# Kernel optimization log

Hardware: AMD Instinct MI355X
Metric: run time of the kernel (lower is better)

The kernel has to match this reference:

```python
import jax, jax.numpy as jnp
import numpy as np

N = 100000      # nodes
E = 1600000     # edges (avg degree 16)
NFEAT = 256
HIDDEN = 256
C = 4           # channels
PC = HIDDEN // C  # per-channel dim = 64
NCLASS = 4
EPS = 1e-12


def setup_inputs() -> dict:
    key = jax.random.key(0)
    ks = jax.random.split(key, 12)
    x = jax.random.normal(ks[0], (N, NFEAT), dtype=jnp.float32)
    row = jax.random.randint(ks[1], (E,), 0, N, dtype=jnp.int64)
    col = jax.random.randint(ks[2], (E,), 0, N, dtype=jnp.int64)
    s = lambda fan_in: 1.0 / np.sqrt(fan_in)
    # NeiborAssigner: Linear(2*nfeat, C) -> Linear(C, C)
    asg_W1 = jax.random.normal(ks[3], (C, 2 * NFEAT), dtype=jnp.float32) * s(2 * NFEAT)
    asg_b1 = jnp.zeros((C,), dtype=jnp.float32)
    asg_W2 = jax.random.normal(ks[4], (C, C), dtype=jnp.float32) * s(C)
    asg_b2 = jnp.zeros((C,), dtype=jnp.float32)
    # DisenLayer: per-channel Linear(nfeat, PC) and conv Linear(PC, PC, bias=False)
    lin_W = jax.random.normal(ks[5], (C, PC, NFEAT), dtype=jnp.float32) * s(NFEAT)
    lin_b = jax.random.normal(ks[6], (C, PC), dtype=jnp.float32) * 0.01
    conv_W = jax.random.normal(ks[7], (C, PC, PC), dtype=jnp.float32) * s(PC)
    bias = jax.random.normal(ks[8], (C, PC), dtype=jnp.float32) * 0.01
    # classifier Linear(hidden, nclass)
    cls_W = jax.random.normal(ks[9], (NCLASS, HIDDEN), dtype=jnp.float32) * s(HIDDEN)
    cls_b = jnp.zeros((NCLASS,), dtype=jnp.float32)
    return {"x": x, "row": row, "col": col,
            "asg_W1": asg_W1, "asg_b1": asg_b1, "asg_W2": asg_W2, "asg_b2": asg_b2,
            "lin_W": lin_W, "lin_b": lin_b, "conv_W": conv_W, "bias": bias,
            "cls_W": cls_W, "cls_b": cls_b}


def reference(x, row, col, asg_W1, asg_b1, asg_W2, asg_b2,
              lin_W, lin_b, conv_W, bias, cls_W, cls_b):
    # --- NeiborAssigner on detached features ---
    xd = jax.lax.stop_gradient(x)
    # cat([x[col], x[row]]) @ W1.T  ==  x[col]@W1a.T + x[row]@W1b.T  (project per node first)
    W1a, W1b = asg_W1[:, :NFEAT], asg_W1[:, NFEAT:]
    proj_a = xd @ W1a.T          # [N, C]
    proj_b = xd @ W1b.T          # [N, C]
    h1 = proj_a[col] + proj_b[row] + asg_b1       # [E, C]
    h2 = h1 @ asg_W2.T + asg_b2                    # [E, C]
    edge_weight = jax.nn.softmax(h2, axis=1)       # [E, C]

    # --- DisenLayer (single layer, layer_num=2) ---
    # per-channel reduce:  z_k = lin_k(x);  c_k = z_k @ conv_W_k.T
    z = jnp.einsum('nf,kpf->nkp', x, lin_W) + lin_b[None]   # [N, C, PC]
    c = jnp.einsum('nkp,kqp->nkq', z, conv_W)               # [N, C, PC]
    # weighted sparse propagate: out[row] += edge_weight[:,k] * c[col]
    msg = c[col] * edge_weight[:, :, None]                  # [E, C, PC]
    out = jax.ops.segment_sum(msg, row, num_segments=N)     # [N, C, PC]
    out = out + bias[None]                                  # per-channel bias
    # F.normalize(p=2, dim=1) per channel
    nrm = jnp.sqrt(jnp.sum(out * out, axis=-1, keepdims=True))
    out = out / jnp.maximum(nrm, EPS)
    h = out.reshape(N, HIDDEN)                              # channel concat
    # dropout is identity in eval mode

    # --- classifier ---
    logits = h @ cls_W.T + cls_b                            # [N, nclass]
    return (h, logits)
```

## Files before the change

### kernel.cpp

```cpp
#include <hip/hip_runtime.h>
#include <hip/hip_bf16.h>

#define N_NODES 100000
#define N_EDGES 1600000
#define BCAP    64
#define EPS     1e-12f

typedef __bf16 bf16x8 __attribute__((ext_vector_type(8)));
typedef float  f32x4  __attribute__((ext_vector_type(4)));

__device__ __forceinline__ unsigned short f2bf(float f){
    union { float f; unsigned int i; } v; v.f = f;
    unsigned int x = v.i;
    return (unsigned short)((x + 0x7fffu + ((x >> 16) & 1u)) >> 16);
}
__device__ __forceinline__ float bits2f(unsigned int u){
    union { unsigned int i; float f; } v; v.i = u; return v.f;
}

__global__ void k_init(int* __restrict__ deg,
                       const float* __restrict__ lin_W,
                       const float* __restrict__ lin_b,
                       const float* __restrict__ conv_W,
                       __bf16* __restrict__ Mbf,
                       float* __restrict__ dvec,
                       const float* __restrict__ asg_W1,
                       const float* __restrict__ x,
                       float* __restrict__ proj_a,
                       float* __restrict__ proj_b){
    int b = blockIdx.x;
    int t = threadIdx.x;
    if (b < 391){
        int i = b * 256 + t;
        if (i < N_NODES) deg[i] = 0;
    } else if (b < 647){
        int id = (b - 391) * 256 + t;
        int f  = id & 255;
        int o  = id >> 8;
        int k  = o >> 6;
        const float* cw = conv_W + o * 64;
        const float* lw = lin_W + k * 64 * 256 + f;
        float s = 0.f;
        #pragma unroll 8
        for (int p = 0; p < 64; ++p) s += cw[p] * lw[p * 256];
        Mbf[id] = (__bf16)s;
        if (f == 0){
            const float* lb = lin_b + k * 64;
            float d = 0.f;
            for (int p = 0; p < 64; ++p) d += lb[p] * cw[p];
            dvec[o] = d;
        }
    } else {
        int p = b - 647;
        int lane = t & 63, wv = t >> 6;
        int nb = p * 128 + wv * 32;
        int l15 = lane & 15, quad = lane >> 4;
        f32x4 accp[2];
        accp[0] = f32x4{0.f, 0.f, 0.f, 0.f};
        accp[1] = f32x4{0.f, 0.f, 0.f, 0.f};
        const float* xg[2];
        #pragma unroll
        for (int mi = 0; mi < 2; ++mi){
            int row = nb + mi * 16 + l15;
            if (row >= N_NODES) row = N_NODES - 1;
            xg[mi] = x + (size_t)row * 256 + quad * 8;
        }
        const float* wrow = asg_W1;
        if (l15 < 4)      wrow = asg_W1 + l15 * 512;
        else if (l15 < 8) wrow = asg_W1 + (l15 - 4) * 512 + 256;
        bool wz = (l15 >= 8);
        for (int k0 = 0; k0 < 256; k0 += 32){
            bf16x8 a[2];
            #pragma unroll
            for (int mi = 0; mi < 2; ++mi){
                float4 lo = *(const float4*)(xg[mi] + k0);
                float4 hi = *(const float4*)(xg[mi] + k0 + 4);
                a[mi][0] = (__bf16)lo.x; a[mi][1] = (__bf16)lo.y;
                a[mi][2] = (__bf16)lo.z; a[mi][3] = (__bf16)lo.w;
                a[mi][4] = (__bf16)hi.x; a[mi][5] = (__bf16)hi.y;
                a[mi][6] = (__bf16)hi.z; a[mi][7] = (__bf16)hi.w;
            }
            bf16x8 bw;
            if (!wz){
                float4 lo = *(const float4*)(wrow + k0 + quad * 8);
                float4 hi = *(const float4*)(wrow + k0 + quad * 8 + 4);
                bw[0] = (__bf16)lo.x; bw[1] = (__bf16)lo.y;
                bw[2] = (__bf16)lo.z; bw[3] = (__bf16)lo.w;
                bw[4] = (__bf16)hi.x; bw[5] = (__bf16)hi.y;
                bw[6] = (__bf16)hi.z; bw[7] = (__bf16)hi.w;
            } else {
                bw[0] = (__bf16)0.f; bw[1] = (__bf16)0.f; bw[2] = (__bf16)0.f; bw[3] = (__bf16)0.f;
                bw[4] = (__bf16)0.f; bw[5] = (__bf16)0.f; bw[6] = (__bf16)0.f; bw[7] = (__bf16)0.f;
            }
            accp[0] = __builtin_amdgcn_mfma_f32_16x16x32_bf16(a[0], bw, accp[0], 0, 0, 0);
            accp[1] = __builtin_amdgcn_mfma_f32_16x16x32_bf16(a[1], bw, accp[1], 0, 0, 0);
        }
        if (l15 < 8){
            #pragma unroll
            for (int mi = 0; mi < 2; ++mi){
                int nrow = nb + mi * 16 + quad * 4;
                #pragma unroll
                for (int r = 0; r < 4; ++r){
                    int node = nrow + r;
                    if (node < N_NODES){
                        float v = accp[mi][r];
                        if (l15 < 4) proj_a[node * 4 + l15] = v;
                        else         proj_b[node * 4 + (l15 - 4)] = v;
                    }
                }
            }
        }
    }
}

__global__ __launch_bounds__(256, 4) void k_ge(const float* __restrict__ x,
                                               const __bf16* __restrict__ Mbf,
                                               const float* __restrict__ dvec,
                                               __bf16* __restrict__ c,
                                               const void* __restrict__ row_raw,
                                               const void* __restrict__ col_raw,
                                               const float* __restrict__ proj_a,
                                               const float* __restrict__ proj_b,
                                               const float* __restrict__ asg_b1,
                                               const float* __restrict__ asg_W2,
                                               const float* __restrict__ asg_b2,
                                               int* __restrict__ deg,
                                               int4* __restrict__ bucket){
    __shared__ int s_is64;
    int b = blockIdx.x;
    int t = threadIdx.x;
    if (b % 5 == 0){
        int gid = b / 5;
        int lane = t & 63, wv = t >> 6;
        int wm = wv & 1, wn = wv >> 1;
        int nb = gid * 64 + wm * 32;
        int ob = wn * 128;
        int l15 = lane & 15, quad = lane >> 4;
        f32x4 acc[2][8];
        #pragma unroll
        for (int mi = 0; mi < 2; ++mi)
            #pragma unroll
            for (int ni = 0; ni < 8; ++ni) acc[mi][ni] = f32x4{0.f, 0.f, 0.f, 0.f};
        const float* xg[2];
        #pragma unroll
        for (int mi = 0; mi < 2; ++mi){
            int row = nb + mi * 16 + l15;
            if (row >= N_NODES) row = N_NODES - 1;
            xg[mi] = x + (size_t)row * 256 + quad * 8;
        }
        for (int k0 = 0; k0 < 256; k0 += 32){
            bf16x8 a[2];
            #pragma unroll
            for (int mi = 0; mi < 2; ++mi){
                float4 lo = *(const float4*)(xg[mi] + k0);
                float4 hi = *(const float4*)(xg[mi] + k0 + 4);
                a[mi][0] = (__bf16)lo.x; a[mi][1] = (__bf16)lo.y;
                a[mi][2] = (__bf16)lo.z; a[mi][3] = (__bf16)lo.w;
                a[mi][4] = (__bf16)hi.x; a[mi][5] = (__bf16)hi.y;
                a[mi][6] = (__bf16)hi.z; a[mi][7] = (__bf16)hi.w;
            }
            #pragma unroll
            for (int ni = 0; ni < 8; ++ni){
                bf16x8 bb = *(const bf16x8*)(Mbf + (size_t)(ob + ni * 16 + l15) * 256 + k0 + quad * 8);
                acc[0][ni] = __builtin_amdgcn_mfma_f32_16x16x32_bf16(a[0], bb, acc[0][ni], 0, 0, 0);
                acc[1][ni] = __builtin_amdgcn_mfma_f32_16x16x32_bf16(a[1], bb, acc[1][ni], 0, 0, 0);
            }
        }
        #pragma unroll
        for (int ni = 0; ni < 8; ++ni){
            int o = ob + ni * 16 + l15;
            float dv = dvec[o];
            #pragma unroll
            for (int mi = 0; mi < 2; ++mi){
                int nrow = nb + mi * 16 + quad * 4;
                #pragma unroll
                for (int r = 0; r < 4; ++r){
                    int node = nrow + r;
                    if (node < N_NODES) c[(size_t)node * 256 + o] = (__bf16)(acc[mi][ni][r] + dv);
                }
            }
        }
    } else {
        int eid = b - b / 5 - 1;
        if (t == 0) s_is64 = 1;
        __syncthreads();
        unsigned v = ((const unsigned*)row_raw)[2 * t + 1] | ((const unsigned*)col_raw)[2 * t + 1];
        if (v) s_is64 = 0;
        __syncthreads();

        int e = eid * 256 + t;
        if (e >= N_EDGES) return;
        int r, cl;
        if (s_is64){
            r  = (int)((const long long*)row_raw)[e];
            cl = (int)((const long long*)col_raw)[e];
        } else {
            r  = ((const int*)row_raw)[e];
            cl = ((const int*)col_raw)[e];
        }
        float4 pa = *(const float4*)(proj_a + (size_t)cl * 4);
        float4 pb = *(const float4*)(proj_b + (size_t)r * 4);
        float h1[4];
        h1[0] = pa.x + pb.x + asg_b1[0];
        h1[1] = pa.y + pb.y + asg_b1[1];
        h1[2] = pa.z + pb.z + asg_b1[2];
        h1[3] = pa.w + pb.w + asg_b1[3];
        float h2[4];
        #pragma unroll
        for (int i = 0; i < 4; ++i){
            float s = asg_b2[i];
            #pragma unroll
            for (int j = 0; j < 4; ++j) s += asg_W2[i * 4 + j] * h1[j];
            h2[i] = s;
        }
        float m = fmaxf(fmaxf(h2[0], h2[1]), fmaxf(h2[2], h2[3]));
        float e0 = __expf(h2[0] - m), e1 = __expf(h2[1] - m);
        float e2 = __expf(h2[2] - m), e3 = __expf(h2[3] - m);
        float inv = 1.f / (e0 + e1 + e2 + e3);
        unsigned b0 = f2bf(e0 * inv), b1 = f2bf(e1 * inv);
        unsigned b2 = f2bf(e2 * inv), b3 = f2bf(e3 * inv);
        int4 rec;
        rec.x = cl;
        rec.y = (int)(b0 | (b1 << 16));
        rec.z = (int)(b2 | (b3 << 16));
        rec.w = 0;
        int pos = atomicAdd(&deg[r], 1);
        if (pos < BCAP) bucket[(size_t)r * BCAP + pos] = rec;
    }
}

__global__ __launch_bounds__(256) void k_node(const __bf16* __restrict__ c,
                                              const int* __restrict__ deg,
                                              const int4* __restrict__ bucket,
                                              const float* __restrict__ bias,
                                              const float* __restrict__ cls_W,
                                              const float* __restrict__ cls_b,
                                              float* __restrict__ out_h,
                                              float* __restrict__ out_logits){
    int wv = __builtin_amdgcn_readfirstlane((int)(threadIdx.x >> 6));
    int l  = threadIdx.x & 63;
    int n  = blockIdx.x * 4 + wv;
    int k2 = l >> 4;

    float4 bi = *(const float4*)(bias  + l * 4);
    float4 w0 = *(const float4*)(cls_W + 0 * 256 + l * 4);
    float4 w1 = *(const float4*)(cls_W + 1 * 256 + l * 4);
    float4 w2 = *(const float4*)(cls_W + 2 * 256 + l * 4);
    float4 w3 = *(const float4*)(cls_W + 3 * 256 + l * 4);

    int dn = deg[n]; if (dn > BCAP) dn = BCAP;
    const int4* rec = bucket + (size_t)n * BCAP;
    const __bf16* cb = c + (size_t)l * 4;

    bool hi2 = (k2 & 2) != 0;
    bool odd = (k2 & 1) != 0;

    float a0 = 0.f, a1 = 0.f, a2 = 0.f, a3 = 0.f;
    #pragma unroll 4
    for (int i = 0; i < dn; ++i){
        int4 rc = rec[i];
        int  ww = hi2 ? rc.z : rc.y;
        unsigned wb = odd ? ((unsigned)ww & 0xffff0000u) : ((unsigned)ww << 16);
        float w = bits2f(wb);
        uint2 vv = *(const uint2*)(cb + (size_t)rc.x * 256);
        a0 += w * bits2f(vv.x << 16);
        a1 += w * bits2f(vv.x & 0xffff0000u);
        a2 += w * bits2f(vv.y << 16);
        a3 += w * bits2f(vv.y & 0xffff0000u);
    }
    a0 += bi.x; a1 += bi.y; a2 += bi.z; a3 += bi.w;

    float ss = a0 * a0 + a1 * a1 + a2 * a2 + a3 * a3;
    ss += __shfl_xor(ss, 1);
    ss += __shfl_xor(ss, 2);
    ss += __shfl_xor(ss, 4);
    ss += __shfl_xor(ss, 8);
    float nrm = fmaxf(sqrtf(ss), EPS);
    float h0 = a0 / nrm, h1 = a1 / nrm, h2 = a2 / nrm, h3 = a3 / nrm;
    *(float4*)(out_h + (size_t)n * 256 + l * 4) = make_float4(h0, h1, h2, h3);

    float p0 = h0 * w0.x + h1 * w0.y + h2 * w0.z + h3 * w0.w;
    float p1 = h0 * w1.x + h1 * w1.y + h2 * w1.z + h3 * w1.w;
    float p2 = h0 * w2.x + h1 * w2.y + h2 * w2.z + h3 * w2.w;
    float p3 = h0 * w3.x + h1 * w3.y + h2 * w3.z + h3 * w3.w;
    #pragma unroll
    for (int off = 1; off < 64; off <<= 1){
        p0 += __shfl_xor(p0, off);
        p1 += __shfl_xor(p1, off);
        p2 += __shfl_xor(p2, off);
        p3 += __shfl_xor(p3, off);
    }
    if (l == 0){
        float4 lg = make_float4(p0 + cls_b[0], p1 + cls_b[1],
                                p2 + cls_b[2], p3 + cls_b[3]);
        *(float4*)(out_logits + (size_t)n * 4) = lg;
    }
}

extern "C" void kernel_launch(void* const* d_in, const int* in_sizes, int n_in,
                              void* d_out, int out_size, void* d_ws, size_t ws_size,
                              hipStream_t stream){
    const float* x       = (const float*)d_in[0];
    const void*  row_raw = d_in[1];
    const void*  col_raw = d_in[2];
    const float* asg_W1  = (const float*)d_in[3];
    const float* asg_b1  = (const float*)d_in[4];
    const float* asg_W2  = (const float*)d_in[5];
    const float* asg_b2  = (const float*)d_in[6];
    const float* lin_W   = (const float*)d_in[7];
    const float* lin_b   = (const float*)d_in[8];
    const float* conv_W  = (const float*)d_in[9];
    const float* bias    = (const float*)d_in[10];
    const float* cls_W   = (const float*)d_in[11];
    const float* cls_b   = (const float*)d_in[12];

    char* ws = (char*)d_ws;
    size_t off = 0;
    auto alloc = [&](size_t bytes) -> void* {
        void* p = ws + off;
        off += (bytes + 255) & ~(size_t)255;
        return p;
    };
    __bf16* c      = (__bf16*)alloc((size_t)N_NODES * 256 * 2);
    int4*   bucket = (int4*)alloc((size_t)N_NODES * BCAP * 16);
    float*  proj_a = (float*)alloc((size_t)N_NODES * 4 * 4);
    float*  proj_b = (float*)alloc((size_t)N_NODES * 4 * 4);
    __bf16* Mbf    = (__bf16*)alloc(65536 * 2);
    float*  dvec   = (float*)alloc(256 * 4);
    int*    deg    = (int*)alloc((size_t)N_NODES * 4);

    float* out_h = (float*)d_out;
    float* out_l = out_h + (size_t)N_NODES * 256;

    hipLaunchKernelGGL(k_init, dim3(647 + (N_NODES + 127) / 128), dim3(256), 0, stream,
                       deg, lin_W, lin_b, conv_W, Mbf, dvec, asg_W1, x, proj_a, proj_b);
    hipLaunchKernelGGL(k_ge, dim3(7813), dim3(256), 0, stream,
                       x, (const __bf16*)Mbf, dvec, c,
                       row_raw, col_raw, proj_a, proj_b, asg_b1, asg_W2, asg_b2,
                       deg, bucket);
    hipLaunchKernelGGL(k_node, dim3(N_NODES / 4), dim3(256), 0, stream,
                       c, deg, bucket, bias, cls_W, cls_b, out_h, out_l);
}
```

Before: 496.8 us.

## Stage x tile in double-buffered LDS and pre-swizzle weight matrix for MFMA loads

The GEMM branch of k_ge now loads each 64-row x tile once per block, converts it to bf16 and stores it in a double-buffered shared-memory tile. This replaces the old scheme where the two waves sharing rows each re-read x from global memory. The next k-slice is prefetched while the MFMAs run. The combined weight matrix is written by k_init in an MFMA-fragment order, so each lane's B load is contiguous and coalesced. The cost is LDS usage and a block barrier per k-step, in a kernel that also carries the edge-processing blocks.

```diff
diff --git a/kernel.cpp b/kernel.cpp
--- a/kernel.cpp
+++ b/kernel.cpp
@@ -22,7 +22,7 @@
                        const float* __restrict__ lin_W,
                        const float* __restrict__ lin_b,
                        const float* __restrict__ conv_W,
-                       __bf16* __restrict__ Mbf,
+                       __bf16* __restrict__ Mp,
                        float* __restrict__ dvec,
                        const float* __restrict__ asg_W1,
                        const float* __restrict__ x,
@@ -43,7 +43,8 @@
         float s = 0.f;
         #pragma unroll 8
         for (int p = 0; p < 64; ++p) s += cw[p] * lw[p * 256];
-        Mbf[id] = (__bf16)s;
+        size_t idx = ((((size_t)(o >> 4) * 8 + (f >> 5)) * 64) + ((f >> 3) & 3) * 16 + (o & 15)) * 8 + (f & 7);
+        Mp[idx] = (__bf16)s;
         if (f == 0){
             const float* lb = lin_b + k * 64;
             float d = 0.f;
@@ -113,8 +114,9 @@
     }
 }
 
+#define ASTRIDE 40
 __global__ __launch_bounds__(256, 4) void k_ge(const float* __restrict__ x,
-                                               const __bf16* __restrict__ Mbf,
+                                               const __bf16* __restrict__ Mp,
                                                const float* __restrict__ dvec,
                                                __bf16* __restrict__ c,
                                                const void* __restrict__ row_raw,
@@ -126,6 +128,7 @@
                                                const float* __restrict__ asg_b2,
                                                int* __restrict__ deg,
                                                int4* __restrict__ bucket){
+    __shared__ __align__(16) __bf16 sA[2][64][ASTRIDE];
     __shared__ int s_is64;
     int b = blockIdx.x;
     int t = threadIdx.x;
@@ -133,46 +136,59 @@
         int gid = b / 5;
         int lane = t & 63, wv = t >> 6;
         int wm = wv & 1, wn = wv >> 1;
-        int nb = gid * 64 + wm * 32;
-        int ob = wn * 128;
+        int nb = gid * 64;
         int l15 = lane & 15, quad = lane >> 4;
         f32x4 acc[2][8];
         #pragma unroll
         for (int mi = 0; mi < 2; ++mi)
             #pragma unroll
             for (int ni = 0; ni < 8; ++ni) acc[mi][ni] = f32x4{0.f, 0.f, 0.f, 0.f};
-        const float* xg[2];
-        #pragma unroll
-        for (int mi = 0; mi < 2; ++mi){
-            int row = nb + mi * 16 + l15;
-            if (row >= N_NODES) row = N_NODES - 1;
-            xg[mi] = x + (size_t)row * 256 + quad * 8;
-        }
-        for (int k0 = 0; k0 < 256; k0 += 32){
+        int srow = t >> 2, scg = t & 3;
+        int grow = nb + srow; if (grow >= N_NODES) grow = N_NODES - 1;
+        const float* gx = x + (size_t)grow * 256 + scg * 8;
+        {
+            float4 lo = *(const float4*)(gx);
+            float4 hi = *(const float4*)(gx + 4);
+            bf16x8 v;
+            v[0] = (__bf16)lo.x; v[1] = (__bf16)lo.y; v[2] = (__bf16)lo.z; v[3] = (__bf16)lo.w;
+            v[4] = (__bf16)hi.x; v[5] = (__bf16)hi.y; v[6] = (__bf16)hi.z; v[7] = (__bf16)hi.w;
+            *(bf16x8*)(&sA[0][srow][scg * 8]) = v;
+        }
+        __syncthreads();
+        const __bf16* bbase = Mp + ((size_t)(wn * 8) * 8) * 512 + lane * 8;
+        int p = 0;
+        for (int ks = 0; ks < 8; ++ks){
+            float4 nlo, nhi;
+            bool pf = (ks < 7);
+            if (pf){
+                nlo = *(const float4*)(gx + (ks + 1) * 32);
+                nhi = *(const float4*)(gx + (ks + 1) * 32 + 4);
+            }
             bf16x8 a[2];
-            #pragma unroll
-            for (int mi = 0; mi < 2; ++mi){
-                float4 lo = *(const float4*)(xg[mi] + k0);
-                float4 hi = *(const float4*)(xg[mi] + k0 + 4);
-                a[mi][0] = (__bf16)lo.x; a[mi][1] = (__bf16)lo.y;
-                a[mi][2] = (__bf16)lo.z; a[mi][3] = (__bf16)lo.w;
-                a[mi][4] = (__bf16)hi.x; a[mi][5] = (__bf16)hi.y;
-                a[mi][6] = (__bf16)hi.z; a[mi][7] = (__bf16)hi.w;
-            }
+            a[0] = *(const bf16x8*)(&sA[p][wm * 32 + l15][quad * 8]);
+            a[1] = *(const bf16x8*)(&sA[p][wm * 32 + 16 + l15][quad * 8]);
             #pragma unroll
             for (int ni = 0; ni < 8; ++ni){
-                bf16x8 bb = *(const bf16x8*)(Mbf + (size_t)(ob + ni * 16 + l15) * 256 + k0 + quad * 8);
+                bf16x8 bb = *(const bf16x8*)(bbase + ((size_t)ni * 8 + ks) * 512);
                 acc[0][ni] = __builtin_amdgcn_mfma_f32_16x16x32_bf16(a[0], bb, acc[0][ni], 0, 0, 0);
                 acc[1][ni] = __builtin_amdgcn_mfma_f32_16x16x32_bf16(a[1], bb, acc[1][ni], 0, 0, 0);
             }
+            if (pf){
+                bf16x8 v;
+                v[0] = (__bf16)nlo.x; v[1] = (__bf16)nlo.y; v[2] = (__bf16)nlo.z; v[3] = (__bf16)nlo.w;
+                v[4] = (__bf16)nhi.x; v[5] = (__bf16)nhi.y; v[6] = (__bf16)nhi.z; v[7] = (__bf16)nhi.w;
+                *(bf16x8*)(&sA[p ^ 1][srow][scg * 8]) = v;
+            }
+            __syncthreads();
+            p ^= 1;
         }
         #pragma unroll
         for (int ni = 0; ni < 8; ++ni){
-            int o = ob + ni * 16 + l15;
+            int o = wn * 128 + ni * 16 + l15;
             float dv = dvec[o];
             #pragma unroll
             for (int mi = 0; mi < 2; ++mi){
-                int nrow = nb + mi * 16 + quad * 4;
+                int nrow = nb + wm * 32 + mi * 16 + quad * 4;
                 #pragma unroll
                 for (int r = 0; r < 4; ++r){
                     int node = nrow + r;
@@ -325,7 +341,7 @@
     int4*   bucket = (int4*)alloc((size_t)N_NODES * BCAP * 16);
     float*  proj_a = (float*)alloc((size_t)N_NODES * 4 * 4);
     float*  proj_b = (float*)alloc((size_t)N_NODES * 4 * 4);
-    __bf16* Mbf    = (__bf16*)alloc(65536 * 2);
+    __bf16* Mp     = (__bf16*)alloc(65536 * 2);
     float*  dvec   = (float*)alloc(256 * 4);
     int*    deg    = (int*)alloc((size_t)N_NODES * 4);
 
@@ -333,9 +349,9 @@
     float* out_l = out_h + (size_t)N_NODES * 256;
 
     hipLaunchKernelGGL(k_init, dim3(647 + (N_NODES + 127) / 128), dim3(256), 0, stream,
-                       deg, lin_W, lin_b, conv_W, Mbf, dvec, asg_W1, x, proj_a, proj_b);
+                       deg, lin_W, lin_b, conv_W, Mp, dvec, asg_W1, x, proj_a, proj_b);
     hipLaunchKernelGGL(k_ge, dim3(7813), dim3(256), 0, stream,
-                       x, (const __bf16*)Mbf, dvec, c,
+                       x, (const __bf16*)Mp, dvec, c,
                        row_raw, col_raw, proj_a, proj_b, asg_b1, asg_W2, asg_b2,
                        deg, bucket);
     hipLaunchKernelGGL(k_node, dim3(N_NODES / 4), dim3(256), 0, stream,
```

After: 460.7 us. 7.3% less time.
